# Optimization experiments

Measured on AMD Instinct MI355X. Metric: run time of the kernel, lower is better.

## Reference

```python
import jax, jax.numpy as jnp
import numpy as np

C = 256
EPS = 1e-5


def setup_inputs() -> dict:
    key = jax.random.key(0)
    ks = jax.random.split(key, 11)
    B, L = 4, 4096
    s = 1.0 / np.sqrt(C)
    inp = {
        'x': jax.random.normal(ks[0], (B, C, L), dtype=jnp.float32),
        'gamma': jnp.ones((C,), jnp.float32),
        'beta': jnp.zeros((C,), jnp.float32),
        'wq': jax.random.normal(ks[1], (C, C), jnp.float32) * s,
        'bq': jax.random.normal(ks[2], (C,), jnp.float32) * 0.01,
        'wk': jax.random.normal(ks[3], (C, C), jnp.float32) * s,
        'bk': jax.random.normal(ks[4], (C,), jnp.float32) * 0.01,
        'wv': jax.random.normal(ks[5], (C, C), jnp.float32) * s,
        'bv': jax.random.normal(ks[6], (C,), jnp.float32) * 0.01,
        'wp': jax.random.normal(ks[7], (C, C), jnp.float32) * s,
        'bp': jax.random.normal(ks[8], (C,), jnp.float32) * 0.01,
    }
    return inp


def reference(x, gamma, beta, wq, bq, wk, bk, wv, bv, wp, bp):
    # BatchNorm1d (training mode): normalize over batch and length dims
    mean = jnp.mean(x, axis=(0, 2), keepdims=True)          # [1,C,1]
    var = jnp.var(x, axis=(0, 2), keepdims=True)            # biased var, as torch BN
    h = (x - mean) * jax.lax.rsqrt(var + EPS)
    h = h * gamma[None, :, None] + beta[None, :, None]

    # 1x1 convs == channel-mixing matmuls: [C_out,C_in] x [B,C_in,L]
    q = jnp.einsum('oc,bcl->bol', wq, h) + bq[None, :, None]
    k = jnp.einsum('oc,bcl->bol', wk, h) + bk[None, :, None]
    v = jnp.einsum('oc,bcl->bol', wv, h) + bv[None, :, None]

    c = q.shape[1]
    scale = jnp.asarray(int(c) ** (-0.5), q.dtype)
    # w[b,i,j] = sum_c q[b,c,i] k[b,c,j]
    w = jnp.einsum('bci,bcj->bij', q, k) * scale
    w = jax.nn.softmax(w, axis=2)
    # torch: h[b,c,i] = sum_j v[b,c,j] * w[b,i,j]
    h = jnp.einsum('bcj,bij->bci', v, w)

    h = jnp.einsum('oc,bcl->bol', wp, h) + bp[None, :, None]
    return x + h
```

## Files before the change

### kernel.cpp

```cpp
#include <hip/hip_runtime.h>
#include <math.h>

typedef unsigned short u16;
typedef unsigned int u32;
typedef short s16x8 __attribute__((ext_vector_type(8)));
typedef float f32x4 __attribute__((ext_vector_type(4)));
typedef float f32x16 __attribute__((ext_vector_type(16)));

static constexpr int Cc = 256;
static constexpr int Ll = 4096;
static constexpr int Bb = 4;

__device__ __forceinline__ u16 f2b(float f) {
    union { float f; unsigned u; } v; v.f = f;
    unsigned r = v.u + 0x7FFF + ((v.u >> 16) & 1);
    return (u16)(r >> 16);
}
__device__ __forceinline__ float b2f(u16 h) {
    union { unsigned u; float f; } v; v.u = ((unsigned)h) << 16; return v.f;
}

__device__ __forceinline__ void gload_lds16(const u16* g, u16* l) {
    __builtin_amdgcn_global_load_lds(
        (const __attribute__((address_space(1))) u32*)g,
        (__attribute__((address_space(3))) u32*)l, 16, 0, 0);
}

__device__ __forceinline__ u32 cvtpk(float lo, float hi) {
    u32 r;
    asm volatile("v_cvt_pk_bf16_f32 %0, %1, %2" : "=v"(r) : "v"(lo), "v"(hi));
    return r;
}

__global__ void k_transpose(const float* __restrict__ x, u16* __restrict__ XT,
                            float* __restrict__ sums) {
    int lt = blockIdx.x, ct = blockIdx.y, b = blockIdx.z, t = threadIdx.x;
    int l0 = lt * 64, c0 = ct * 64;
    __shared__ u16 tile[64][65];
    __shared__ float red[2][4][64];
    int ll = t & 63, cb = t >> 6;
    #pragma unroll
    for (int rep = 0; rep < 16; rep++) {
        int cl = cb * 16 + rep;
        tile[cl][ll] = f2b(x[(size_t)(b * Cc + c0 + cl) * Ll + l0 + ll]);
    }
    __syncthreads();
    int cl2 = t & 63, lb = t >> 6;
    float s = 0.f, s2 = 0.f;
    #pragma unroll
    for (int rep = 0; rep < 16; rep++) {
        int ll2 = lb * 16 + rep;
        u16 hv = tile[cl2][ll2];
        XT[(size_t)(b * Ll + l0 + ll2) * Cc + c0 + cl2] = hv;
        float v = b2f(hv);
        s += v; s2 += v * v;
    }
    red[0][lb][cl2] = s;
    red[1][lb][cl2] = s2;
    __syncthreads();
    if (t < 64) {
        float ss = red[0][0][t] + red[0][1][t] + red[0][2][t] + red[0][3][t];
        float ss2 = red[1][0][t] + red[1][1][t] + red[1][2][t] + red[1][3][t];
        atomicAdd(&sums[c0 + t], ss);
        atomicAdd(&sums[256 + c0 + t], ss2);
    }
}

__global__ void k_fold(const float* __restrict__ wq, const float* __restrict__ bq,
                       const float* __restrict__ wk, const float* __restrict__ bk,
                       const float* __restrict__ wv, const float* __restrict__ bv,
                       const float* __restrict__ wp,
                       const float* __restrict__ gamma, const float* __restrict__ beta,
                       const float* __restrict__ sums,
                       u16* __restrict__ Wqkv, float* __restrict__ biasQKV,
                       u16* __restrict__ Wp16) {
    int m = blockIdx.x, t = threadIdx.x;
    if (m >= 768) {
        int row = m - 768;
        Wp16[row * Cc + t] = f2b(wp[row * Cc + t]);
        return;
    }
    const float inv_n = 1.f / (Bb * Ll);
    float mean = sums[t] * inv_n;
    float var  = sums[256 + t] * inv_n - mean * mean;
    float rstd = rsqrtf(var + 1e-5f);
    float a  = gamma[t] * rstd;
    float cB = beta[t] - mean * a;
    int type = m >> 8, row = m & 255;
    const float* W  = (type == 0) ? wq : (type == 1) ? wk : wv;
    const float* bs = (type == 0) ? bq : (type == 1) ? bk : bv;
    float wval = W[row * Cc + t];
    float s2 = (type == 0) ? 0.09016844005556021f : 1.0f;
    Wqkv[m * Cc + t] = f2b(wval * a * s2);
    __shared__ float rs[256];
    rs[t] = wval * cB;
    __syncthreads();
    for (int off = 128; off > 0; off >>= 1) {
        if (t < off) rs[t] += rs[t + off];
        __syncthreads();
    }
    if (t == 0) biasQKV[m] = (bs[row] + rs[0]) * s2;
}

__launch_bounds__(256, 2)
__global__ void k_qkv(const u16* __restrict__ XT, const u16* __restrict__ Wqkv,
                      const float* __restrict__ biasQKV,
                      u16* __restrict__ QT, u16* __restrict__ KT, u16* __restrict__ V) {
    int ly = blockIdx.x, b = blockIdx.y;
    int t = threadIdx.x, w = t >> 6, lane = t & 63;
    int l16 = lane & 15, quad = lane >> 4;
    int l0 = ly * 64;
    __shared__ u16 Xs[64][264];
    {
        int row = t >> 2, chunk = t & 3;
        const u16* src = XT + (size_t)(b * Ll + l0 + row) * Cc + chunk * 64;
        u16* dst = &Xs[row][chunk * 64];
        #pragma unroll
        for (int u = 0; u < 8; u++)
            *(uint4*)(dst + u * 8) = *(const uint4*)(src + u * 8);
    }
    __syncthreads();
    for (int ox = 0; ox < 12; ox++) {
        int o0 = ox * 64;
        s16x8 af[8];
        {
            const u16* wrow = Wqkv + (size_t)(o0 + w * 16 + l16) * Cc + quad * 8;
            #pragma unroll
            for (int ks = 0; ks < 8; ks++) af[ks] = *(const s16x8*)(wrow + ks * 32);
        }
        f32x4 acc[4];
        #pragma unroll
        for (int ns = 0; ns < 4; ns++)
            #pragma unroll
            for (int r = 0; r < 4; r++) acc[ns][r] = 0.f;
        #pragma unroll
        for (int ks = 0; ks < 8; ks++) {
            #pragma unroll
            for (int ns = 0; ns < 4; ns++) {
                s16x8 bf = *(const s16x8*)(&Xs[ns * 16 + l16][ks * 32 + quad * 8]);
                acc[ns] = __builtin_amdgcn_mfma_f32_16x16x32_bf16(af[ks], bf, acc[ns], 0, 0, 0);
            }
        }
        int obase = o0 + w * 16 + quad * 4;
        float bias[4];
        #pragma unroll
        for (int r = 0; r < 4; r++) bias[r] = biasQKV[obase + r];
        #pragma unroll
        for (int ns = 0; ns < 4; ns++) {
            int l = l0 + ns * 16 + l16;
            if (ox < 8) {
                u16* dstbase = (ox < 4) ? QT : KT;
                int oo = obase - ((ox < 4) ? 0 : 256);
                ushort4 pk;
                pk.x = f2b(acc[ns][0] + bias[0]);
                pk.y = f2b(acc[ns][1] + bias[1]);
                pk.z = f2b(acc[ns][2] + bias[2]);
                pk.w = f2b(acc[ns][3] + bias[3]);
                *(ushort4*)(dstbase + (size_t)(b * Ll + l) * Cc + oo) = pk;
            } else {
                #pragma unroll
                for (int r = 0; r < 4; r++) {
                    int o = obase + r - 512;
                    V[(size_t)(b * Cc + o) * Ll + l] = f2b(acc[ns][r] + bias[r]);
                }
            }
        }
    }
}

__launch_bounds__(512, 2)
__global__ void k_attn(const u16* __restrict__ QT, const u16* __restrict__ KT,
                       const u16* __restrict__ V, u16* __restrict__ Opart,
                       float* __restrict__ Lpart) {
    int id = blockIdx.x;
    int xcd = id & 7, local = id >> 3;
    int b = xcd >> 1;
    int u = local * 2 + (xcd & 1);
    int itile = u >> 1;
    int jh = u & 1;
    int t = threadIdx.x, w = t >> 6, lane = t & 63;
    int iw = w & 3, jsub = w >> 2;
    int l31 = lane & 31, hi = lane >> 5;

    __shared__ u16 lds_buf[65536];
    __shared__ float Lred[2][4][32];

    s16x8 qf[16];
    {
        const u16* qbase = QT + (size_t)(b * Ll + itile * 128 + iw * 32 + l31) * Cc + hi * 8;
        #pragma unroll
        for (int ks = 0; ks < 16; ks++) qf[ks] = *(const s16x8*)(qbase + ks * 16);
    }

    const u16* kcur = KT + (size_t)(b * Ll + jh * 2048 + l31) * Cc + hi * 8;
    const u16* vcur = V + (size_t)(b * Cc + l31) * Ll + jh * 2048 + hi * 8;
    int kwo = w * 16;
    size_t vwo = (size_t)((w >> 2) * 32) * Ll + (w & 3) * 16;
    int ldw = w * 512;

#define STAGE_K(c) { u16* kd = lds_buf + (c) * 16384 + ldw;  \
    gload_lds16(kcur + kwo,        kd);          \
    gload_lds16(kcur + kwo + 128,  kd + 4096);   \
    gload_lds16(kcur + kwo + 8192, kd + 8192);   \
    gload_lds16(kcur + kwo + 8320, kd + 12288);  \
    kcur += 64 * Cc; }
#define STAGE_V(c) { u16* vd = lds_buf + 32768 + (c) * 16384 + ldw;  \
    gload_lds16(vcur + vwo,          vd);          \
    gload_lds16(vcur + vwo + 262144, vd + 4096);   \
    gload_lds16(vcur + vwo + 524288, vd + 8192);   \
    gload_lds16(vcur + vwo + 786432, vd + 12288);  \
    vcur += 64; }

    STAGE_K(0); STAGE_V(0); STAGE_K(1); STAGE_V(1);

    f32x16 of[8];
    #pragma unroll
    for (int ct = 0; ct < 8; ct++)
        #pragma unroll
        for (int r = 0; r < 16; r++) of[ct][r] = 0.f;
    float lsum = 0.f;

    asm volatile("s_waitcnt vmcnt(12)" ::: "memory");
    __builtin_amdgcn_s_barrier();

    int aoff = jsub * 8192 + lane * 8;
    int boff = jsub * 1024 + lane * 8;

    for (int it = 0; it < 32; it++) {
        const u16* KaC = lds_buf + (it & 1) * 16384;
        const u16* VbC = lds_buf + 32768 + (it & 1) * 16384;

        f32x16 s0, s1;
        #pragma unroll
        for (int r = 0; r < 16; r++) { s0[r] = 0.f; s1[r] = 0.f; }
        __builtin_amdgcn_s_setprio(1);
        #pragma unroll
        for (int ks = 0; ks < 16; ks += 2) {
            s16x8 kf0 = *(const s16x8*)(KaC + aoff + ks * 512);
            s16x8 kf1 = *(const s16x8*)(KaC + aoff + ks * 512 + 512);
            s0 = __builtin_amdgcn_mfma_f32_32x32x16_bf16(kf0, qf[ks], s0, 0, 0, 0);
            s1 = __builtin_amdgcn_mfma_f32_32x32x16_bf16(kf1, qf[ks + 1], s1, 0, 0, 0);
        }
        __builtin_amdgcn_s_setprio(0);

        float p[16];
        #pragma unroll
        for (int r = 0; r < 16; r++) {
            p[r] = __builtin_amdgcn_exp2f(s0[r] + s1[r]);
            lsum += p[r];
        }
        u32 paw[2][4];
        #pragma unroll
        for (int js = 0; js < 2; js++) {
            int o = js * 8;
            u32 a0 = cvtpk(p[o + 0], p[o + 1]);
            u32 b0 = cvtpk(p[o + 4], p[o + 5]);
            u32 a1 = cvtpk(p[o + 2], p[o + 3]);
            u32 b1 = cvtpk(p[o + 6], p[o + 7]);
            asm volatile("v_permlane32_swap_b32 %0, %1" : "+v"(a0), "+v"(b0));
            asm volatile("v_permlane32_swap_b32 %0, %1" : "+v"(a1), "+v"(b1));
            paw[js][0] = a0; paw[js][1] = a1; paw[js][2] = b0; paw[js][3] = b1;
        }

        asm volatile("s_waitcnt lgkmcnt(0)" ::: "memory");
        if (it < 31) asm volatile("s_waitcnt vmcnt(8)" ::: "memory");
        else         asm volatile("s_waitcnt vmcnt(0)" ::: "memory");
        __builtin_amdgcn_s_barrier();
        if (it < 30) STAGE_K(it & 1);

        __builtin_amdgcn_s_setprio(1);
        #pragma unroll
        for (int js = 0; js < 2; js++) {
            union { u32 u[4]; s16x8 v; } pa;
            pa.u[0] = paw[js][0]; pa.u[1] = paw[js][1];
            pa.u[2] = paw[js][2]; pa.u[3] = paw[js][3];
            #pragma unroll
            for (int ct = 0; ct < 8; ct++) {
                s16x8 bf = *(const s16x8*)(VbC + ct * 2048 + boff + js * 512);
                of[ct] = __builtin_amdgcn_mfma_f32_32x32x16_bf16(pa.v, bf, of[ct], 0, 0, 0);
            }
        }
        __builtin_amdgcn_s_setprio(0);

        if (it < 31) {
            asm volatile("s_waitcnt lgkmcnt(0)" ::: "memory");
            if (it < 30) asm volatile("s_waitcnt vmcnt(8)" ::: "memory");
            else         asm volatile("s_waitcnt vmcnt(4)" ::: "memory");
            __builtin_amdgcn_s_barrier();
            if (it < 30) STAGE_V(it & 1);
        }
    }
#undef STAGE_K
#undef STAGE_V

    lsum += __shfl_xor(lsum, 32);
    if (lane < 32) Lred[jsub][iw][l31] = lsum;
    __syncthreads();
    int mi0 = (jh * 4 + b) * Ll + itile * 128;
    if (jsub == 0 && lane < 32)
        Lpart[mi0 + iw * 32 + l31] = Lred[0][iw][l31] + Lred[1][iw][l31];

    float* Om = (float*)lds_buf;
    if (jsub == 1) {
        #pragma unroll
        for (int ct = 0; ct < 8; ct++)
            #pragma unroll
            for (int r = 0; r < 16; r++)
                Om[((iw * 8 + ct) * 16 + r) * 64 + lane] = of[ct][r];
    }
    __syncthreads();
    if (jsub == 0) {
        #pragma unroll
        for (int ct = 0; ct < 8; ct++)
            #pragma unroll
            for (int r = 0; r < 16; r++) {
                float val = of[ct][r] + Om[((iw * 8 + ct) * 16 + r) * 64 + lane];
                int rl = (r & 3) + 8 * (r >> 2) + 4 * hi;
                Opart[(size_t)(mi0 + iw * 32 + rl) * 256 + ct * 32 + l31] = f2b(val);
            }
    }
}

__global__ void k_merge(const u16* __restrict__ Opart, const float* __restrict__ Lpart,
                        u16* __restrict__ OT) {
    int id = blockIdx.x, t = threadIdx.x;
    int b = id >> 6, itile = id & 63;
    int row = t >> 2, seg = t & 3;
    size_t i0 = ((size_t)(0 + b) * 64 + itile) * 64 + row;
    size_t i1 = ((size_t)(4 + b) * 64 + itile) * 64 + row;
    float inv = 1.f / (Lpart[i0] + Lpart[i1]);
    const u16* p0 = Opart + i0 * 256 + seg * 64;
    const u16* p1 = Opart + i1 * 256 + seg * 64;
    u16* dst = OT + (size_t)(b * Ll + itile * 64 + row) * Cc + seg * 64;
    #pragma unroll
    for (int k = 0; k < 8; k++) {
        ushort4 a0 = *(const ushort4*)(p0 + k * 8 + 0);
        ushort4 b0 = *(const ushort4*)(p0 + k * 8 + 4);
        ushort4 a1 = *(const ushort4*)(p1 + k * 8 + 0);
        ushort4 b1 = *(const ushort4*)(p1 + k * 8 + 4);
        ushort4 oA, oB;
        oA.x = f2b((b2f(a0.x) + b2f(a1.x)) * inv);
        oA.y = f2b((b2f(a0.y) + b2f(a1.y)) * inv);
        oA.z = f2b((b2f(a0.z) + b2f(a1.z)) * inv);
        oA.w = f2b((b2f(a0.w) + b2f(a1.w)) * inv);
        oB.x = f2b((b2f(b0.x) + b2f(b1.x)) * inv);
        oB.y = f2b((b2f(b0.y) + b2f(b1.y)) * inv);
        oB.z = f2b((b2f(b0.z) + b2f(b1.z)) * inv);
        oB.w = f2b((b2f(b0.w) + b2f(b1.w)) * inv);
        *(ushort4*)(dst + k * 8 + 0) = oA;
        *(ushort4*)(dst + k * 8 + 4) = oB;
    }
}

__launch_bounds__(256, 2)
__global__ void k_proj(const u16* __restrict__ OT, const u16* __restrict__ Opart,
                       const float* __restrict__ Lpart, int fused,
                       const u16* __restrict__ Wp16,
                       const float* __restrict__ bp, const float* __restrict__ x,
                       float* __restrict__ out) {
    int ly = blockIdx.x, b = blockIdx.y;
    int t = threadIdx.x, w = t >> 6, lane = t & 63;
    int l16 = lane & 15, quad = lane >> 4;
    int l0 = ly * 64;
    __shared__ u16 Os[64][264];
    {
        int row = t >> 2, chunk = t & 3;
        u16* dst = &Os[row][chunk * 64];
        if (fused) {
            size_t i0 = ((size_t)(0 + b) * Ll + l0 + row);
            size_t i1 = ((size_t)(4 + b) * Ll + l0 + row);
            float inv = 1.f / (Lpart[i0] + Lpart[i1]);
            const u16* p0 = Opart + i0 * 256 + chunk * 64;
            const u16* p1 = Opart + i1 * 256 + chunk * 64;
            #pragma unroll
            for (int k = 0; k < 8; k++) {
                ushort4 a0 = *(const ushort4*)(p0 + k * 8 + 0);
                ushort4 b0 = *(const ushort4*)(p0 + k * 8 + 4);
                ushort4 a1 = *(const ushort4*)(p1 + k * 8 + 0);
                ushort4 b1 = *(const ushort4*)(p1 + k * 8 + 4);
                ushort4 oA, oB;
                oA.x = f2b((b2f(a0.x) + b2f(a1.x)) * inv);
                oA.y = f2b((b2f(a0.y) + b2f(a1.y)) * inv);
                oA.z = f2b((b2f(a0.z) + b2f(a1.z)) * inv);
                oA.w = f2b((b2f(a0.w) + b2f(a1.w)) * inv);
                oB.x = f2b((b2f(b0.x) + b2f(b1.x)) * inv);
                oB.y = f2b((b2f(b0.y) + b2f(b1.y)) * inv);
                oB.z = f2b((b2f(b0.z) + b2f(b1.z)) * inv);
                oB.w = f2b((b2f(b0.w) + b2f(b1.w)) * inv);
                *(ushort4*)(dst + k * 8 + 0) = oA;
                *(ushort4*)(dst + k * 8 + 4) = oB;
            }
        } else {
            const u16* src = OT + (size_t)(b * Ll + l0 + row) * Cc + chunk * 64;
            #pragma unroll
            for (int u = 0; u < 8; u++)
                *(uint4*)(dst + u * 8) = *(const uint4*)(src + u * 8);
        }
    }
    __syncthreads();
    for (int ox = 0; ox < 4; ox++) {
        int o0 = ox * 64;
        s16x8 af[8];
        {
            const u16* wrow = Wp16 + (size_t)(o0 + w * 16 + l16) * Cc + quad * 8;
            #pragma unroll
            for (int ks = 0; ks < 8; ks++) af[ks] = *(const s16x8*)(wrow + ks * 32);
        }
        f32x4 acc[4];
        #pragma unroll
        for (int ns = 0; ns < 4; ns++)
            #pragma unroll
            for (int r = 0; r < 4; r++) acc[ns][r] = 0.f;
        #pragma unroll
        for (int ks = 0; ks < 8; ks++) {
            #pragma unroll
            for (int ns = 0; ns < 4; ns++) {
                s16x8 bf = *(const s16x8*)(&Os[ns * 16 + l16][ks * 32 + quad * 8]);
                acc[ns] = __builtin_amdgcn_mfma_f32_16x16x32_bf16(af[ks], bf, acc[ns], 0, 0, 0);
            }
        }
        int ob = o0 + w * 16 + quad * 4;
        float bias[4];
        #pragma unroll
        for (int r = 0; r < 4; r++) bias[r] = bp[ob + r];
        #pragma unroll
        for (int ns = 0; ns < 4; ns++) {
            #pragma unroll
            for (int r = 0; r < 4; r++) {
                int o = ob + r;
                int l = l0 + ns * 16 + l16;
                size_t idx = (size_t)(b * Cc + o) * Ll + l;
                out[idx] = x[idx] + bias[r] + acc[ns][r];
            }
        }
    }
}

extern "C" void kernel_launch(void* const* d_in, const int* in_sizes, int n_in,
                              void* d_out, int out_size, void* d_ws, size_t ws_size,
                              hipStream_t stream) {
    const float* x     = (const float*)d_in[0];
    const float* gamma = (const float*)d_in[1];
    const float* beta  = (const float*)d_in[2];
    const float* wq    = (const float*)d_in[3];
    const float* bq    = (const float*)d_in[4];
    const float* wk    = (const float*)d_in[5];
    const float* bk    = (const float*)d_in[6];
    const float* wv    = (const float*)d_in[7];
    const float* bv    = (const float*)d_in[8];
    const float* wp    = (const float*)d_in[9];
    const float* bp    = (const float*)d_in[10];
    float* out = (float*)d_out;
    char* ws = (char*)d_ws;

    float* sums    = (float*)(ws + 0);
    float* biasQKV = (float*)(ws + 2048);
    u16*   Wqkv    = (u16*)(ws + 8192);
    u16*   Wp16    = (u16*)(ws + 401408);
    u16*   XT      = (u16*)(ws + 532480);
    u16*   QT      = (u16*)(ws + 8921088);
    u16*   KT      = (u16*)(ws + 17309696);
    u16*   V       = (u16*)(ws + 25698304);
    u16*   OT      = XT;

    const size_t opart_off = 34086912;
    const size_t lpart_off = opart_off + 16777216;
    const size_t needed    = lpart_off + 131072;
    int fused = (ws_size >= needed) ? 1 : 0;
    u16*   Opart = fused ? (u16*)(ws + opart_off) : (u16*)d_out;
    float* Lpart = (float*)(ws + (fused ? lpart_off : opart_off));

    (void)hipMemsetAsync(sums, 0, 2048, stream);
    k_transpose<<<dim3(64, 4, 4), 256, 0, stream>>>(x, XT, sums);
    k_fold<<<1024, 256, 0, stream>>>(wq, bq, wk, bk, wv, bv, wp, gamma, beta,
                                     sums, Wqkv, biasQKV, Wp16);
    k_qkv<<<dim3(64, 4), 256, 0, stream>>>(XT, Wqkv, biasQKV, QT, KT, V);
    k_attn<<<256, 512, 0, stream>>>(QT, KT, V, Opart, Lpart);
    if (!fused)
        k_merge<<<256, 256, 0, stream>>>(Opart, Lpart, OT);
    k_proj<<<dim3(64, 4), 256, 0, stream>>>(OT, Opart, Lpart, fused,
                                            Wp16, bp, x, out);
}
```

Baseline: 224.4 us.

## Halve attention waves, each wave computes two 32-row query tiles

The attention kernel drops from 512 to 256 threads per block. Each wave now holds two query fragments, so every K fragment read from LDS feeds two MFMAs and every V fragment feeds two PV MFMAs, which halves LDS traffic per MFMA. Staging loops now issue 8 async loads per wave, and the hand-tuned waitcnt/setprio sequencing is replaced with plain __syncthreads. The cost is roughly doubled accumulator registers per wave, fewer waves to hide latency, and coarser synchronization.

```diff
diff --git a/kernel.cpp b/kernel.cpp
--- a/kernel.cpp
+++ b/kernel.cpp
@@ -168,7 +168,7 @@
     }
 }
 
-__launch_bounds__(512, 2)
+__launch_bounds__(256, 1)
 __global__ void k_attn(const u16* __restrict__ QT, const u16* __restrict__ KT,
                        const u16* __restrict__ V, u16* __restrict__ Opart,
                        float* __restrict__ Lpart) {
@@ -179,49 +179,52 @@
     int itile = u >> 1;
     int jh = u & 1;
     int t = threadIdx.x, w = t >> 6, lane = t & 63;
-    int iw = w & 3, jsub = w >> 2;
+    int iw = w & 1, jsub = w >> 1;
     int l31 = lane & 31, hi = lane >> 5;
 
     __shared__ u16 lds_buf[65536];
     __shared__ float Lred[2][4][32];
 
-    s16x8 qf[16];
+    s16x8 qf0[16], qf1[16];
     {
-        const u16* qbase = QT + (size_t)(b * Ll + itile * 128 + iw * 32 + l31) * Cc + hi * 8;
-        #pragma unroll
-        for (int ks = 0; ks < 16; ks++) qf[ks] = *(const s16x8*)(qbase + ks * 16);
+        const u16* qb0 = QT + (size_t)(b * Ll + itile * 128 + iw * 64 + l31) * Cc + hi * 8;
+        const u16* qb1 = qb0 + 32 * Cc;
+        #pragma unroll
+        for (int ks = 0; ks < 16; ks++) qf0[ks] = *(const s16x8*)(qb0 + ks * 16);
+        #pragma unroll
+        for (int ks = 0; ks < 16; ks++) qf1[ks] = *(const s16x8*)(qb1 + ks * 16);
     }
 
     const u16* kcur = KT + (size_t)(b * Ll + jh * 2048 + l31) * Cc + hi * 8;
     const u16* vcur = V + (size_t)(b * Cc + l31) * Ll + jh * 2048 + hi * 8;
-    int kwo = w * 16;
-    size_t vwo = (size_t)((w >> 2) * 32) * Ll + (w & 3) * 16;
-    int ldw = w * 512;
-
-#define STAGE_K(c) { u16* kd = lds_buf + (c) * 16384 + ldw;  \
-    gload_lds16(kcur + kwo,        kd);          \
-    gload_lds16(kcur + kwo + 128,  kd + 4096);   \
-    gload_lds16(kcur + kwo + 8192, kd + 8192);   \
-    gload_lds16(kcur + kwo + 8320, kd + 12288);  \
+
+#define STAGE_K(c) { u16* kd = lds_buf + (c) * 16384;                          \
+    _Pragma("unroll")                                                          \
+    for (int R = 0; R < 8; R++) {                                              \
+        int g = R * 4 + w;                                                     \
+        gload_lds16(kcur + (size_t)((g >> 4) * 32) * Cc + (g & 15) * 16,       \
+                    kd + g * 512);                                             \
+    }                                                                          \
     kcur += 64 * Cc; }
-#define STAGE_V(c) { u16* vd = lds_buf + 32768 + (c) * 16384 + ldw;  \
-    gload_lds16(vcur + vwo,          vd);          \
-    gload_lds16(vcur + vwo + 262144, vd + 4096);   \
-    gload_lds16(vcur + vwo + 524288, vd + 8192);   \
-    gload_lds16(vcur + vwo + 786432, vd + 12288);  \
+#define STAGE_V(c) { u16* vd = lds_buf + 32768 + (c) * 16384;                  \
+    _Pragma("unroll")                                                          \
+    for (int R = 0; R < 8; R++) {                                              \
+        int g = R * 4 + w;                                                     \
+        gload_lds16(vcur + (size_t)((g >> 2) * 32) * Ll + (g & 3) * 16,        \
+                    vd + g * 512);                                             \
+    }                                                                          \
     vcur += 64; }
 
     STAGE_K(0); STAGE_V(0); STAGE_K(1); STAGE_V(1);
 
-    f32x16 of[8];
+    f32x16 of0[8], of1[8];
     #pragma unroll
     for (int ct = 0; ct < 8; ct++)
         #pragma unroll
-        for (int r = 0; r < 16; r++) of[ct][r] = 0.f;
-    float lsum = 0.f;
-
-    asm volatile("s_waitcnt vmcnt(12)" ::: "memory");
-    __builtin_amdgcn_s_barrier();
+        for (int r = 0; r < 16; r++) { of0[ct][r] = 0.f; of1[ct][r] = 0.f; }
+    float lsum0 = 0.f, lsum1 = 0.f;
+
+    __syncthreads();
 
     int aoff = jsub * 8192 + lane * 8;
     int boff = jsub * 1024 + lane * 8;
@@ -233,80 +236,98 @@
         f32x16 s0, s1;
         #pragma unroll
         for (int r = 0; r < 16; r++) { s0[r] = 0.f; s1[r] = 0.f; }
-        __builtin_amdgcn_s_setprio(1);
-        #pragma unroll
-        for (int ks = 0; ks < 16; ks += 2) {
-            s16x8 kf0 = *(const s16x8*)(KaC + aoff + ks * 512);
-            s16x8 kf1 = *(const s16x8*)(KaC + aoff + ks * 512 + 512);
-            s0 = __builtin_amdgcn_mfma_f32_32x32x16_bf16(kf0, qf[ks], s0, 0, 0, 0);
-            s1 = __builtin_amdgcn_mfma_f32_32x32x16_bf16(kf1, qf[ks + 1], s1, 0, 0, 0);
-        }
-        __builtin_amdgcn_s_setprio(0);
-
-        float p[16];
-        #pragma unroll
-        for (int r = 0; r < 16; r++) {
-            p[r] = __builtin_amdgcn_exp2f(s0[r] + s1[r]);
-            lsum += p[r];
-        }
-        u32 paw[2][4];
+        #pragma unroll
+        for (int ks = 0; ks < 16; ks++) {
+            s16x8 kf = *(const s16x8*)(KaC + aoff + ks * 512);
+            s0 = __builtin_amdgcn_mfma_f32_32x32x16_bf16(kf, qf0[ks], s0, 0, 0, 0);
+            s1 = __builtin_amdgcn_mfma_f32_32x32x16_bf16(kf, qf1[ks], s1, 0, 0, 0);
+        }
+
+        u32 paw0[2][4], paw1[2][4];
+        {
+            float p[16];
+            #pragma unroll
+            for (int r = 0; r < 16; r++) {
+                p[r] = __builtin_amdgcn_exp2f(s0[r]);
+                lsum0 += p[r];
+            }
+            #pragma unroll
+            for (int js = 0; js < 2; js++) {
+                int o = js * 8;
+                u32 a0 = cvtpk(p[o + 0], p[o + 1]);
+                u32 b0 = cvtpk(p[o + 4], p[o + 5]);
+                u32 a1 = cvtpk(p[o + 2], p[o + 3]);
+                u32 b1 = cvtpk(p[o + 6], p[o + 7]);
+                asm volatile("v_permlane32_swap_b32 %0, %1" : "+v"(a0), "+v"(b0));
+                asm volatile("v_permlane32_swap_b32 %0, %1" : "+v"(a1), "+v"(b1));
+                paw0[js][0] = a0; paw0[js][1] = a1; paw0[js][2] = b0; paw0[js][3] = b1;
+            }
+            #pragma unroll
+            for (int r = 0; r < 16; r++) {
+                p[r] = __builtin_amdgcn_exp2f(s1[r]);
+                lsum1 += p[r];
+            }
+            #pragma unroll
+            for (int js = 0; js < 2; js++) {
+                int o = js * 8;
+                u32 a0 = cvtpk(p[o + 0], p[o + 1]);
+                u32 b0 = cvtpk(p[o + 4], p[o + 5]);
+                u32 a1 = cvtpk(p[o + 2], p[o + 3]);
+                u32 b1 = cvtpk(p[o + 6], p[o + 7]);
+                asm volatile("v_permlane32_swap_b32 %0, %1" : "+v"(a0), "+v"(b0));
+                asm volatile("v_permlane32_swap_b32 %0, %1" : "+v"(a1), "+v"(b1));
+                paw1[js][0] = a0; paw1[js][1] = a1; paw1[js][2] = b0; paw1[js][3] = b1;
+            }
+        }
+
+        __syncthreads();
+        if (it < 30) STAGE_K(it & 1);
+
         #pragma unroll
         for (int js = 0; js < 2; js++) {
-            int o = js * 8;
-            u32 a0 = cvtpk(p[o + 0], p[o + 1]);
-            u32 b0 = cvtpk(p[o + 4], p[o + 5]);
-            u32 a1 = cvtpk(p[o + 2], p[o + 3]);
-            u32 b1 = cvtpk(p[o + 6], p[o + 7]);
-            asm volatile("v_permlane32_swap_b32 %0, %1" : "+v"(a0), "+v"(b0));
-            asm volatile("v_permlane32_swap_b32 %0, %1" : "+v"(a1), "+v"(b1));
-            paw[js][0] = a0; paw[js][1] = a1; paw[js][2] = b0; paw[js][3] = b1;
-        }
-
-        asm volatile("s_waitcnt lgkmcnt(0)" ::: "memory");
-        if (it < 31) asm volatile("s_waitcnt vmcnt(8)" ::: "memory");
-        else         asm volatile("s_waitcnt vmcnt(0)" ::: "memory");
-        __builtin_amdgcn_s_barrier();
-        if (it < 30) STAGE_K(it & 1);
-
-        __builtin_amdgcn_s_setprio(1);
-        #pragma unroll
-        for (int js = 0; js < 2; js++) {
-            union { u32 u[4]; s16x8 v; } pa;
-            pa.u[0] = paw[js][0]; pa.u[1] = paw[js][1];
-            pa.u[2] = paw[js][2]; pa.u[3] = paw[js][3];
+            union { u32 u[4]; s16x8 v; } pa0, pa1;
+            pa0.u[0] = paw0[js][0]; pa0.u[1] = paw0[js][1];
+            pa0.u[2] = paw0[js][2]; pa0.u[3] = paw0[js][3];
+            pa1.u[0] = paw1[js][0]; pa1.u[1] = paw1[js][1];
+            pa1.u[2] = paw1[js][2]; pa1.u[3] = paw1[js][3];
             #pragma unroll
             for (int ct = 0; ct < 8; ct++) {
                 s16x8 bf = *(const s16x8*)(VbC + ct * 2048 + boff + js * 512);
-                of[ct] = __builtin_amdgcn_mfma_f32_32x32x16_bf16(pa.v, bf, of[ct], 0, 0, 0);
-            }
-        }
-        __builtin_amdgcn_s_setprio(0);
+                of0[ct] = __builtin_amdgcn_mfma_f32_32x32x16_bf16(pa0.v, bf, of0[ct], 0, 0, 0);
+                of1[ct] = __builtin_amdgcn_mfma_f32_32x32x16_bf16(pa1.v, bf, of1[ct], 0, 0, 0);
+            }
+        }
 
         if (it < 31) {
-            asm volatile("s_waitcnt lgkmcnt(0)" ::: "memory");
-            if (it < 30) asm volatile("s_waitcnt vmcnt(8)" ::: "memory");
-            else         asm volatile("s_waitcnt vmcnt(4)" ::: "memory");
-            __builtin_amdgcn_s_barrier();
+            __syncthreads();
             if (it < 30) STAGE_V(it & 1);
         }
     }
 #undef STAGE_K
 #undef STAGE_V
 
-    lsum += __shfl_xor(lsum, 32);
-    if (lane < 32) Lred[jsub][iw][l31] = lsum;
+    lsum0 += __shfl_xor(lsum0, 32);
+    lsum1 += __shfl_xor(lsum1, 32);
+    if (lane < 32) {
+        Lred[jsub][iw * 2 + 0][l31] = lsum0;
+        Lred[jsub][iw * 2 + 1][l31] = lsum1;
+    }
     __syncthreads();
     int mi0 = (jh * 4 + b) * Ll + itile * 128;
-    if (jsub == 0 && lane < 32)
-        Lpart[mi0 + iw * 32 + l31] = Lred[0][iw][l31] + Lred[1][iw][l31];
+    if (jsub == 0 && lane < 32) {
+        Lpart[mi0 + iw * 64 + l31]      = Lred[0][iw * 2 + 0][l31] + Lred[1][iw * 2 + 0][l31];
+        Lpart[mi0 + iw * 64 + 32 + l31] = Lred[0][iw * 2 + 1][l31] + Lred[1][iw * 2 + 1][l31];
+    }
 
     float* Om = (float*)lds_buf;
     if (jsub == 1) {
         #pragma unroll
         for (int ct = 0; ct < 8; ct++)
             #pragma unroll
-            for (int r = 0; r < 16; r++)
-                Om[((iw * 8 + ct) * 16 + r) * 64 + lane] = of[ct][r];
+            for (int r = 0; r < 16; r++) {
+                Om[(((iw * 2 + 0) * 8 + ct) * 16 + r) * 64 + lane] = of0[ct][r];
+                Om[(((iw * 2 + 1) * 8 + ct) * 16 + r) * 64 + lane] = of1[ct][r];
+            }
     }
     __syncthreads();
     if (jsub == 0) {
@@ -314,9 +335,11 @@
         for (int ct = 0; ct < 8; ct++)
             #pragma unroll
             for (int r = 0; r < 16; r++) {
-                float val = of[ct][r] + Om[((iw * 8 + ct) * 16 + r) * 64 + lane];
                 int rl = (r & 3) + 8 * (r >> 2) + 4 * hi;
-                Opart[(size_t)(mi0 + iw * 32 + rl) * 256 + ct * 32 + l31] = f2b(val);
+                float v0 = of0[ct][r] + Om[(((iw * 2 + 0) * 8 + ct) * 16 + r) * 64 + lane];
+                Opart[(size_t)(mi0 + iw * 64 + rl) * 256 + ct * 32 + l31] = f2b(v0);
+                float v1 = of1[ct][r] + Om[(((iw * 2 + 1) * 8 + ct) * 16 + r) * 64 + lane];
+                Opart[(size_t)(mi0 + iw * 64 + 32 + rl) * 256 + ct * 32 + l31] = f2b(v1);
             }
     }
 }
@@ -475,7 +498,7 @@
     k_fold<<<1024, 256, 0, stream>>>(wq, bq, wk, bk, wv, bv, wp, gamma, beta,
                                      sums, Wqkv, biasQKV, Wp16);
     k_qkv<<<dim3(64, 4), 256, 0, stream>>>(XT, Wqkv, biasQKV, QT, KT, V);
-    k_attn<<<256, 512, 0, stream>>>(QT, KT, V, Opart, Lpart);
+    k_attn<<<256, 256, 0, stream>>>(QT, KT, V, Opart, Lpart);
     if (!fused)
         k_merge<<<256, 256, 0, stream>>>(Opart, Lpart, OT);
     k_proj<<<dim3(64, 4), 256, 0, stream>>>(OT, Opart, Lpart, fused,
```

New measurement: 300.2 us. 1.34x slower.
